# Performance work log

Hardware: AMD Instinct MI355X
Metric: run time of the kernel (lower is better)

## Reference

```python
import jax, jax.numpy as jnp
import numpy as np

NH, WIN = 8, 7  # num_head, window


def _ln(x, w, b, eps=1e-6):
    mu = x.mean(-1, keepdims=True)
    var = ((x - mu) ** 2).mean(-1, keepdims=True)
    return (x - mu) / jnp.sqrt(var + eps) * w + b


def _dwconv(x, w, b):
    # x: (B,C,H,W), w: (C,1,7,7) depthwise, pad 3
    y = jax.lax.conv_general_dilated(
        x, w, (1, 1), ((3, 3), (3, 3)),
        dimension_numbers=('NCHW', 'OIHW', 'NCHW'),
        feature_group_count=x.shape[1])
    return y + b[None, :, None, None]


def _forward(x, x_e, norm_w, norm_b, norme_w, norme_b,
             rr1_w, rr1_b, rr2_w, rr2_b, rr3_w, rr3_b, conv_w, conv_b,
             la1_w, la1_b, la2_w, la2_b, lac1_w, lac1_b, lac2_w, lac2_b,
             fc1_w, fc2_w, la3_w, la3_b,
             kv_w, kv_b, q_w, q_b, proj_w, proj_b, proje_w, proje_b):
    B, H, W, C = x.shape
    hd = C // NH // 2  # head dim of half-width attention
    xn = _ln(x, norm_w, norm_b)
    xen = _ln(x_e, norme_w, norme_b)

    # local_rr branch: gated depthwise-conv mixing (C channels)
    rr1 = xn @ rr1_w + rr1_b
    rr2 = xn @ rr2_w + rr2_b
    rr2 = _dwconv(rr2.transpose(0, 3, 1, 2), conv_w, conv_b).transpose(0, 2, 3, 1)
    rr2 = rr2 @ rr3_w + rr3_b
    local_rr = rr1 * rr2  # (B,H,W,C)

    # LocalAttentionRGBT branch -> (B,H,W,C//2)
    rgb = (xn @ la1_w + la1_b).transpose(0, 3, 1, 2)   # (B,C/2,H,W)
    t = (xen @ la2_w + la2_b).transpose(0, 3, 1, 2)
    co = _dwconv(rgb * t, lac1_w, lac1_b)
    di = _dwconv(jnp.abs(rgb - t), lac2_w, lac2_b)
    co_di = jnp.concatenate([co, di], 1).transpose(0, 2, 3, 1)  # (B,H,W,C)
    amap = co_di.mean(-1, keepdims=True)                         # (B,H,W,1)
    dot = (amap * co_di).sum((1, 2), keepdims=True)              # (B,1,1,C)
    n1 = jnp.sqrt((amap ** 2).sum((1, 2), keepdims=True))        # (B,1,1,1)
    n2 = jnp.sqrt((co_di ** 2).sum((1, 2), keepdims=True))       # (B,1,1,C)
    cos = dot / (n1 * n2 + 1e-6)
    attc = jax.nn.sigmoid(jax.nn.gelu(cos @ fc1_w, approximate=False) @ fc2_w)
    local_rx = (co_di * attc) @ la3_w + la3_b  # (B,H,W,C/2)

    # global pooled attention: 49 queries vs full H*W keys, C/2 wide
    kv = (xn @ kv_w + kv_b).reshape(B, H * W, 2, NH, hd).transpose(2, 0, 3, 1, 4)
    k, v = kv[0], kv[1]  # (B,NH,HW,hd)
    rx = jnp.concatenate([xn, xen], -1)  # (B,H,W,3C/2)
    ph, pw = H // WIN, W // WIN  # exact adaptive pool (H,W divisible by 7)
    rx_pool = rx.reshape(B, WIN, ph, WIN, pw, rx.shape[-1]).mean((2, 4))  # (B,7,7,3C/2)
    q = (rx_pool @ q_w + q_b).reshape(B, WIN * WIN, NH, hd).transpose(0, 2, 1, 3)
    attn = jax.nn.softmax((q * hd ** -0.5) @ k.transpose(0, 1, 3, 2), axis=-1)  # (B,NH,49,HW)
    g = (attn @ v).reshape(B, NH, WIN, WIN, hd).transpose(0, 1, 4, 2, 3).reshape(B, C // 2, WIN, WIN)
    g = jax.image.resize(g, (B, C // 2, H, W), method='bilinear').transpose(0, 2, 3, 1)

    xc = jnp.concatenate([local_rr, g, local_rx], -1)  # (B,H,W,2C)
    out_e = xc @ proje_w + proje_b  # (B,H,W,C/2)
    out = xc @ proj_w + proj_b      # (B,H,W,C)
    return out, out_e


def setup_inputs() -> dict:
    C = 128
    B, H, W = 8, 112, 112
    ks = iter(jax.random.split(jax.random.key(0), 24))

    def w(shape):
        return jax.random.normal(next(ks), shape, jnp.float32) * 0.05

    inp = {
        'x': jax.random.normal(next(ks), (B, H, W, C), jnp.float32),
        'x_e': jax.random.normal(next(ks), (B, H, W, C // 2), jnp.float32),
        'norm_w': jnp.ones((C,), jnp.float32), 'norm_b': jnp.zeros((C,), jnp.float32),
        'norme_w': jnp.ones((C // 2,), jnp.float32), 'norme_b': jnp.zeros((C // 2,), jnp.float32),
        'rr1_w': w((C, C)), 'rr1_b': jnp.zeros((C,), jnp.float32),
        'rr2_w': w((C, C)), 'rr2_b': jnp.zeros((C,), jnp.float32),
        'rr3_w': w((C, C)), 'rr3_b': jnp.zeros((C,), jnp.float32),
        'conv_w': w((C, 1, 7, 7)), 'conv_b': jnp.zeros((C,), jnp.float32),
        'la1_w': w((C, C // 2)), 'la1_b': jnp.zeros((C // 2,), jnp.float32),
        'la2_w': w((C // 2, C // 2)), 'la2_b': jnp.zeros((C // 2,), jnp.float32),
        'lac1_w': w((C // 2, 1, 7, 7)), 'lac1_b': jnp.zeros((C // 2,), jnp.float32),
        'lac2_w': w((C // 2, 1, 7, 7)), 'lac2_b': jnp.zeros((C // 2,), jnp.float32),
        'fc1_w': w((C, C // 8)), 'fc2_w': w((C // 8, C)),
        'la3_w': w((C, C // 2)), 'la3_b': jnp.zeros((C // 2,), jnp.float32),
        'kv_w': w((C, C)), 'kv_b': jnp.zeros((C,), jnp.float32),
        'q_w': w((3 * C // 2, C // 2)), 'q_b': jnp.zeros((C // 2,), jnp.float32),
        'proj_w': w((2 * C, C)), 'proj_b': jnp.zeros((C,), jnp.float32),
        'proje_w': w((2 * C, C // 2)), 'proje_b': jnp.zeros((C // 2,), jnp.float32),
    }
    return inp


def reference(x, x_e, norm_w, norm_b, norme_w, norme_b,
              rr1_w, rr1_b, rr2_w, rr2_b, rr3_w, rr3_b, conv_w, conv_b,
              la1_w, la1_b, la2_w, la2_b, lac1_w, lac1_b, lac2_w, lac2_b,
              fc1_w, fc2_w, la3_w, la3_b,
              kv_w, kv_b, q_w, q_b, proj_w, proj_b, proje_w, proje_b):
    return _forward(x, x_e, norm_w, norm_b, norme_w, norme_b,
                    rr1_w, rr1_b, rr2_w, rr2_b, rr3_w, rr3_b, conv_w, conv_b,
                    la1_w, la1_b, la2_w, la2_b, lac1_w, lac1_b, lac2_w, lac2_b,
                    fc1_w, fc2_w, la3_w, la3_b,
                    kv_w, kv_b, q_w, q_b, proj_w, proj_b, proje_w, proje_b)
```

## Files before the change

### kernel.cpp

```cpp
#include <hip/hip_runtime.h>
#include <math.h>

#define N_POS 100352
#define HW    12544

typedef unsigned short bf16_t;
typedef __attribute__((ext_vector_type(8))) short bf16x8;
typedef __attribute__((ext_vector_type(4))) float f32x4;

__device__ __forceinline__ bf16_t f2b(float f){
  unsigned u = __builtin_bit_cast(unsigned, f);
  unsigned r = (u + 0x7fffu + ((u >> 16) & 1u)) >> 16;
  return (bf16_t)r;
}
__device__ __forceinline__ float b2f(bf16_t h){
  unsigned u = ((unsigned)h) << 16;
  return __builtin_bit_cast(float, u);
}
__device__ __forceinline__ float blo(unsigned u){
  return __builtin_bit_cast(float, u << 16);
}
__device__ __forceinline__ float bhi(unsigned u){
  return __builtin_bit_cast(float, u & 0xffff0000u);
}

__global__ void zero_kernel(float* p, int n){
  int i = blockIdx.x*256 + threadIdx.x;
  if (i < n) p[i] = 0.f;
}

struct WJob { const float* src; bf16_t* dst; int K; int ldw; int n0; };
struct WJobs { WJob j[14]; };
__global__ void wtrans_kernel(WJobs js){
  WJob job = js.j[blockIdx.x];
  int t = threadIdx.x;
  int n = t & 63, k0 = t >> 6;
  for (int k = k0; k < job.K; k += 4)
    job.dst[(size_t)n*job.K + k] = f2b(job.src[(size_t)k*job.ldw + job.n0 + n]);
}

__global__ __launch_bounds__(256) void ln128_kernel(const float* __restrict__ in,
    const float* __restrict__ w, const float* __restrict__ b, bf16_t* __restrict__ out){
  int row  = blockIdx.x*4 + (threadIdx.x >> 6);
  int lane = threadIdx.x & 63;
  const float* p = in + (size_t)row*128;
  float2 v = *(const float2*)(p + lane*2);
  float s = v.x + v.y;
  #pragma unroll
  for (int o = 1; o < 64; o <<= 1) s += __shfl_xor(s, o);
  float mu = s * (1.0f/128.0f);
  float dx = v.x - mu, dy = v.y - mu;
  float q = dx*dx + dy*dy;
  #pragma unroll
  for (int o = 1; o < 64; o <<= 1) q += __shfl_xor(q, o);
  float rs = rsqrtf(q * (1.0f/128.0f) + 1e-6f);
  int c = lane*2;
  ushort2 o2;
  o2.x = f2b(dx*rs*w[c]   + b[c]);
  o2.y = f2b(dy*rs*w[c+1] + b[c+1]);
  *(ushort2*)(out + (size_t)row*128 + c) = o2;
}

__global__ __launch_bounds__(256) void ln64_kernel(const float* __restrict__ in,
    const float* __restrict__ w, const float* __restrict__ b, bf16_t* __restrict__ out){
  int row  = blockIdx.x*4 + (threadIdx.x >> 6);
  int lane = threadIdx.x & 63;
  float v = in[(size_t)row*64 + lane];
  float s = v;
  #pragma unroll
  for (int o = 1; o < 64; o <<= 1) s += __shfl_xor(s, o);
  float mu = s * (1.0f/64.0f);
  float d = v - mu;
  float q = d*d;
  #pragma unroll
  for (int o = 1; o < 64; o <<= 1) q += __shfl_xor(q, o);
  float rs = rsqrtf(q * (1.0f/64.0f) + 1e-6f);
  out[(size_t)row*64 + lane] = f2b(d*rs*w[lane] + b[lane]);
}

struct MTile {
  const bf16_t* Wt;
  const float* bias;
  void* out;
  const bf16_t* mult;
  int ldo; int ldm; int out_fp32;
};
struct MGemmParams {
  const bf16_t* A; const float* scale;
  int lda; int K; int rowsPerB;
  MTile tiles[8];
};

__global__ __launch_bounds__(256) void mgemm(MGemmParams p){
  __shared__ short As[128*72];
  __shared__ short Ws[64*72];
  const int tid = threadIdx.x;
  const MTile tile = p.tiles[blockIdx.x];
  const int row0 = blockIdx.y * 128;
  const int lane = tid & 63, wv = tid >> 6;
  const int wm = wv * 32;
  const int fm = lane & 15;
  const int quad = lane >> 4;
  f32x4 acc[2][4];
  #pragma unroll
  for (int mi = 0; mi < 2; mi++)
    #pragma unroll
    for (int ni = 0; ni < 4; ni++) acc[mi][ni] = (f32x4)0.f;
  const float* scale = p.scale ? (p.scale + (size_t)(row0 / p.rowsPerB) * p.K) : (const float*)0;

  const int sr = tid & 127, sq = tid >> 7;
  const int wn = tid & 63,  wq = tid >> 6;

  for (int k0 = 0; k0 < p.K; k0 += 64) {
    {
      const bf16_t* src = p.A + (size_t)(row0 + sr)*p.lda + k0 + sq*32;
      short* dst = &As[sr*72 + sq*32];
      if (!scale) {
        #pragma unroll
        for (int i = 0; i < 4; i++)
          *(uint4*)(dst + i*8) = *(const uint4*)(src + i*8);
      } else {
        const float* sc = scale + k0 + sq*32;
        #pragma unroll
        for (int i = 0; i < 32; i++) dst[i] = (short)f2b(b2f(src[i]) * sc[i]);
      }
    }
    {
      const bf16_t* src = tile.Wt + (size_t)wn*p.K + k0 + wq*16;
      short* dst = &Ws[wn*72 + wq*16];
      *(uint4*)dst       = *(const uint4*)src;
      *(uint4*)(dst + 8) = *(const uint4*)(src + 8);
    }
    __syncthreads();
    #pragma unroll
    for (int ks = 0; ks < 2; ks++) {
      int kb = ks*32 + quad*8;
      bf16x8 af0 = *(const bf16x8*)&As[(wm + fm)*72 + kb];
      bf16x8 af1 = *(const bf16x8*)&As[(wm + 16 + fm)*72 + kb];
      bf16x8 bfr[4];
      #pragma unroll
      for (int ni = 0; ni < 4; ni++) bfr[ni] = *(const bf16x8*)&Ws[(ni*16 + fm)*72 + kb];
      #pragma unroll
      for (int ni = 0; ni < 4; ni++) {
        acc[0][ni] = __builtin_amdgcn_mfma_f32_16x16x32_bf16(af0, bfr[ni], acc[0][ni], 0, 0, 0);
        acc[1][ni] = __builtin_amdgcn_mfma_f32_16x16x32_bf16(af1, bfr[ni], acc[1][ni], 0, 0, 0);
      }
    }
    __syncthreads();
  }
  #pragma unroll
  for (int mi = 0; mi < 2; mi++) {
    #pragma unroll
    for (int ni = 0; ni < 4; ni++) {
      int col = ni*16 + fm;
      float bias = tile.bias[col];
      #pragma unroll
      for (int r = 0; r < 4; r++) {
        int row = row0 + wm + mi*16 + quad*4 + r;
        float val = acc[mi][ni][r] + bias;
        if (tile.mult) val *= b2f(tile.mult[(size_t)row*tile.ldm + col]);
        if (tile.out_fp32) ((float*)tile.out)[(size_t)row*tile.ldo + col] = val;
        else ((bf16_t*)tile.out)[(size_t)row*tile.ldo + col] = f2b(val);
      }
    }
  }
}

__global__ __launch_bounds__(256) void dwconv128_kernel(const bf16_t* __restrict__ in,
    const float* __restrict__ cw, const float* __restrict__ cb, bf16_t* __restrict__ out){
  __shared__ float wsm[49*128];
  int t = threadIdx.x;
  for (int i = t; i < 6272; i += 256) {
    int ch = i / 49, k = i % 49;
    wsm[k*128 + ch] = cw[i];
  }
  __syncthreads();
  int c = (t & 63) * 2;
  int wv = t >> 6;
  int blk = blockIdx.x;
  int xs = blk % 14; int tmp = blk / 14;
  int yg = tmp % 14; int b = tmp / 14;
  int y0 = yg*8 + wv*2;
  int x0 = xs*8;
  float2 bias; bias.x = cb[c]; bias.y = cb[c+1];
  float2 acc0[8], acc1[8];
  #pragma unroll
  for (int i = 0; i < 8; i++) { acc0[i] = bias; acc1[i] = bias; }
  for (int r = 0; r < 8; r++) {
    int yy = y0 + r - 3;
    if ((unsigned)yy >= 112u) continue;
    const bf16_t* row = in + ((size_t)(b*112+yy)*112)*128 + c;
    unsigned u[14];
    #pragma unroll
    for (int i = 0; i < 14; i++) {
      int xx = x0 + i - 3;
      u[i] = ((unsigned)xx < 112u) ? *(const unsigned*)(row + (size_t)xx*128) : 0u;
    }
    float va[14], vb[14];
    #pragma unroll
    for (int i = 0; i < 14; i++) { va[i] = blo(u[i]); vb[i] = bhi(u[i]); }
    if (r < 7) {
      #pragma unroll
      for (int kx = 0; kx < 7; kx++) {
        float2 w = *(const float2*)&wsm[(r*7+kx)*128 + c];
        #pragma unroll
        for (int i = 0; i < 8; i++) {
          acc0[i].x = fmaf(w.x, va[i+kx], acc0[i].x);
          acc0[i].y = fmaf(w.y, vb[i+kx], acc0[i].y);
        }
      }
    }
    if (r >= 1) {
      #pragma unroll
      for (int kx = 0; kx < 7; kx++) {
        float2 w = *(const float2*)&wsm[((r-1)*7+kx)*128 + c];
        #pragma unroll
        for (int i = 0; i < 8; i++) {
          acc1[i].x = fmaf(w.x, va[i+kx], acc1[i].x);
          acc1[i].y = fmaf(w.y, vb[i+kx], acc1[i].y);
        }
      }
    }
  }
  size_t r0 = (size_t)(b*112+y0)*112 + x0;
  #pragma unroll
  for (int i = 0; i < 8; i++) {
    unsigned o0 = (unsigned)f2b(acc0[i].x) | ((unsigned)f2b(acc0[i].y) << 16);
    unsigned o1 = (unsigned)f2b(acc1[i].x) | ((unsigned)f2b(acc1[i].y) << 16);
    *(unsigned*)(out + (r0+i)*128 + c)       = o0;
    *(unsigned*)(out + (r0+112+i)*128 + c)   = o1;
  }
}

__global__ __launch_bounds__(256) void dwconv_codi_kernel(
    const bf16_t* __restrict__ rgb, const bf16_t* __restrict__ tb,
    const float* __restrict__ w1, const float* __restrict__ b1,
    const float* __restrict__ w2, const float* __restrict__ b2,
    bf16_t* __restrict__ out){
  __shared__ float wsm[49*128];
  int t = threadIdx.x;
  for (int i = t; i < 3136; i += 256) {
    int ch = i / 49, k = i % 49;
    wsm[k*128 + ch]      = w1[i];
    wsm[k*128 + 64 + ch] = w2[i];
  }
  __syncthreads();
  int c = (t & 31) * 2;
  int yrow = t >> 5;
  int blk = blockIdx.x;
  int xs = blk % 14; int tmp = blk / 14;
  int yg = tmp % 14; int b = tmp / 14;
  int y = yg*8 + yrow;
  int x0 = xs*8;
  float2 bco; bco.x = b1[c]; bco.y = b1[c+1];
  float2 bdi; bdi.x = b2[c]; bdi.y = b2[c+1];
  float2 acc_co[8], acc_di[8];
  #pragma unroll
  for (int i = 0; i < 8; i++) { acc_co[i] = bco; acc_di[i] = bdi; }
  for (int r = 0; r < 7; r++) {
    int yy = y + r - 3;
    if ((unsigned)yy >= 112u) continue;
    const bf16_t* rrow = rgb + ((size_t)(b*112+yy)*112)*64 + c;
    const bf16_t* trow = tb  + ((size_t)(b*112+yy)*112)*64 + c;
    unsigned ru[14], tu[14];
    #pragma unroll
    for (int i = 0; i < 14; i++) {
      int xx = x0 + i - 3;
      bool ok = (unsigned)xx < 112u;
      ru[i] = ok ? *(const unsigned*)(rrow + (size_t)xx*64) : 0u;
      tu[i] = ok ? *(const unsigned*)(trow + (size_t)xx*64) : 0u;
    }
    float p0[14], p1[14], d0[14], d1[14];
    #pragma unroll
    for (int i = 0; i < 14; i++) {
      float a0 = blo(ru[i]), a1 = bhi(ru[i]);
      float t0 = blo(tu[i]), t1 = bhi(tu[i]);
      p0[i] = a0*t0; p1[i] = a1*t1;
      d0[i] = fabsf(a0-t0); d1[i] = fabsf(a1-t1);
    }
    #pragma unroll
    for (int kx = 0; kx < 7; kx++) {
      int k = r*7+kx;
      float2 wc = *(const float2*)&wsm[k*128 + c];
      float2 wd = *(const float2*)&wsm[k*128 + 64 + c];
      #pragma unroll
      for (int i = 0; i < 8; i++) {
        acc_co[i].x = fmaf(wc.x, p0[i+kx], acc_co[i].x);
        acc_co[i].y = fmaf(wc.y, p1[i+kx], acc_co[i].y);
        acc_di[i].x = fmaf(wd.x, d0[i+kx], acc_di[i].x);
        acc_di[i].y = fmaf(wd.y, d1[i+kx], acc_di[i].y);
      }
    }
  }
  size_t r0 = (size_t)(b*112+y)*112 + x0;
  #pragma unroll
  for (int i = 0; i < 8; i++) {
    unsigned oc = (unsigned)f2b(acc_co[i].x) | ((unsigned)f2b(acc_co[i].y) << 16);
    unsigned od = (unsigned)f2b(acc_di[i].x) | ((unsigned)f2b(acc_di[i].y) << 16);
    *(unsigned*)(out + (r0+i)*128 + c)      = oc;
    *(unsigned*)(out + (r0+i)*128 + 64 + c) = od;
  }
}

__global__ __launch_bounds__(256) void reduce_kernel(const bf16_t* __restrict__ codi,
    float* __restrict__ dotb, float* __restrict__ n1sq, float* __restrict__ n2sq){
  int blk = blockIdx.x;
  int b = blk / 49, seg = blk % 49;
  int lane = threadIdx.x & 63, w = threadIdx.x >> 6;
  int c = lane*2;
  float d0=0,d1=0,s0=0,s1=0,a1=0;
  for (int i = 0; i < 64; i++) {
    int row = b*HW + seg*256 + w*64 + i;
    ushort2 v2 = *(const ushort2*)(codi + (size_t)row*128 + c);
    float vx = b2f(v2.x), vy = b2f(v2.y);
    float rs = vx + vy;
    #pragma unroll
    for (int o = 1; o < 64; o <<= 1) rs += __shfl_xor(rs, o);
    float amap = rs * (1.0f/128.0f);
    d0 += amap*vx; d1 += amap*vy;
    s0 += vx*vx;   s1 += vy*vy;
    if (lane == 0) a1 += amap*amap;
  }
  atomicAdd(&dotb[b*128+c],   d0); atomicAdd(&dotb[b*128+c+1], d1);
  atomicAdd(&n2sq[b*128+c],   s0); atomicAdd(&n2sq[b*128+c+1], s1);
  if (lane == 0) atomicAdd(&n1sq[b], a1);
}

__global__ __launch_bounds__(128) void attc_kernel(const float* __restrict__ dotb,
    const float* __restrict__ n1sq, const float* __restrict__ n2sq,
    const float* __restrict__ fc1, const float* __restrict__ fc2, float* __restrict__ attc){
  __shared__ float scos[128];
  __shared__ float sh[16];
  int t = threadIdx.x;
  int b = blockIdx.x;
  {
    float n1 = sqrtf(n1sq[b]);
    float n2 = sqrtf(n2sq[b*128+t]);
    scos[t] = dotb[b*128+t] / (n1*n2 + 1e-6f);
  }
  __syncthreads();
  if (t < 16) {
    float h = 0;
    for (int c = 0; c < 128; c++) h += scos[c]*fc1[c*16+t];
    sh[t] = h * 0.5f * (1.0f + erff(h*0.70710678118654752f));
  }
  __syncthreads();
  {
    float a = 0;
    for (int j = 0; j < 16; j++) a += sh[j]*fc2[j*128+t];
    attc[b*128+t] = 1.0f/(1.0f + __expf(-a));
  }
}

__global__ void pool_kernel(const bf16_t* __restrict__ xn, const bf16_t* __restrict__ xen,
                            float* __restrict__ pool){
  int cellb = blockIdx.x;
  int py = blockIdx.y;
  int c = threadIdx.x;
  int b = cellb / 49, cell = cellb % 49;
  int wy = cell / 7, wx = cell % 7;
  float s = 0;
  for (int i = py*2; i < py*2+2; i++)
    for (int j = 0; j < 16; j++) {
      int y = wy*16+i, x = wx*16+j;
      size_t row = (size_t)(b*112+y)*112 + x;
      s += (c < 128) ? b2f(xn[row*128 + c]) : b2f(xen[row*64 + (c-128)]);
    }
  atomicAdd(&pool[(size_t)cellb*192 + c], s);
}

__global__ void qproj_kernel(const float* __restrict__ pool, const float* __restrict__ qw,
                             const float* __restrict__ qb, float* __restrict__ qbuf){
  int cellb = blockIdx.x;
  int j = threadIdx.x;
  float s = qb[j];
  for (int c = 0; c < 192; c++)
    s += pool[(size_t)cellb*192 + c] * (1.0f/256.0f) * qw[c*64 + j];
  qbuf[(size_t)cellb*64 + j] = s * 0.35355339059327373f;
}

__global__ __launch_bounds__(256) void attn_kernel(const float* __restrict__ qbuf,
    const bf16_t* __restrict__ kv, float* __restrict__ part){
  __shared__ float qs[392];
  __shared__ float ks[256*8];
  __shared__ float vs[256*8];
  int t = threadIdx.x;
  int blk = blockIdx.x;
  int b = blk >> 6, nh = (blk >> 3) & 7, sp = blk & 7;
  for (int i = t; i < 392; i += 256)
    qs[i] = qbuf[(size_t)(b*49 + (i>>3))*64 + nh*8 + (i&7)];
  __syncthreads();
  int lane = t & 63, w = t >> 6;
  int qq = lane < 49 ? lane : 0;
  float4 qa = *(const float4*)&qs[qq*8];
  float4 qb4 = *(const float4*)&qs[qq*8+4];
  float m = -1e30f, l = 0.f;
  float4 acca = make_float4(0,0,0,0), accb = make_float4(0,0,0,0);
  const int base = sp * 1568;
  for (int c0 = 0; c0 < 1568; c0 += 256) {
    int cnt = 1568 - c0 < 256 ? 1568 - c0 : 256;
    __syncthreads();
    if (t < cnt) {
      size_t rb = ((size_t)(b*HW + base + c0 + t))*128 + nh*8;
      uint4 kr = *(const uint4*)(kv + rb);
      uint4 vr = *(const uint4*)(kv + rb + 64);
      const bf16_t* kp = (const bf16_t*)&kr;
      const bf16_t* vp = (const bf16_t*)&vr;
      #pragma unroll
      for (int j = 0; j < 8; j++) { ks[t*8+j] = b2f(kp[j]); vs[t*8+j] = b2f(vp[j]); }
    }
    __syncthreads();
    int s0 = w*64;
    int n = cnt - s0; if (n > 64) n = 64;
    for (int i = 0; i < n; i += 16) {
      float s[16];
      #pragma unroll
      for (int j = 0; j < 16; j++) {
        const float* kp = &ks[(s0+i+j)*8];
        float4 ka = *(const float4*)kp, kb = *(const float4*)(kp+4);
        s[j] = qa.x*ka.x + qa.y*ka.y + qa.z*ka.z + qa.w*ka.w
             + qb4.x*kb.x + qb4.y*kb.y + qb4.z*kb.z + qb4.w*kb.w;
      }
      float t8[8];
      #pragma unroll
      for (int j = 0; j < 8; j++) t8[j] = fmaxf(s[2*j], s[2*j+1]);
      float t4a = fmaxf(t8[0], t8[1]), t4b = fmaxf(t8[2], t8[3]);
      float t4c = fmaxf(t8[4], t8[5]), t4d = fmaxf(t8[6], t8[7]);
      float mx = fmaxf(fmaxf(t4a, t4b), fmaxf(t4c, t4d));
      float mn = fmaxf(m, mx);
      float corr = __expf(m - mn);
      float p[16];
      #pragma unroll
      for (int j = 0; j < 16; j++) p[j] = __expf(s[j] - mn);
      float u8[8];
      #pragma unroll
      for (int j = 0; j < 8; j++) u8[j] = p[2*j] + p[2*j+1];
      float u4a = u8[0]+u8[1], u4b = u8[2]+u8[3], u4c = u8[4]+u8[5], u4d = u8[6]+u8[7];
      float lsum = (u4a+u4b) + (u4c+u4d);
      l = fmaf(l, corr, lsum);
      float4 sva = make_float4(0,0,0,0), svb = make_float4(0,0,0,0);
      #pragma unroll
      for (int j = 0; j < 16; j++) {
        const float* vp = &vs[(s0+i+j)*8];
        float4 va = *(const float4*)vp, vb = *(const float4*)(vp+4);
        sva.x = fmaf(p[j], va.x, sva.x); sva.y = fmaf(p[j], va.y, sva.y);
        sva.z = fmaf(p[j], va.z, sva.z); sva.w = fmaf(p[j], va.w, sva.w);
        svb.x = fmaf(p[j], vb.x, svb.x); svb.y = fmaf(p[j], vb.y, svb.y);
        svb.z = fmaf(p[j], vb.z, svb.z); svb.w = fmaf(p[j], vb.w, svb.w);
      }
      acca.x = fmaf(acca.x, corr, sva.x); acca.y = fmaf(acca.y, corr, sva.y);
      acca.z = fmaf(acca.z, corr, sva.z); acca.w = fmaf(acca.w, corr, sva.w);
      accb.x = fmaf(accb.x, corr, svb.x); accb.y = fmaf(accb.y, corr, svb.y);
      accb.z = fmaf(accb.z, corr, svb.z); accb.w = fmaf(accb.w, corr, svb.w);
      m = mn;
    }
  }
  if (lane < 49) {
    size_t idx = ((size_t)(blk*4 + w)*49 + lane)*10;
    part[idx] = m; part[idx+1] = l;
    part[idx+2] = acca.x; part[idx+3] = acca.y; part[idx+4] = acca.z; part[idx+5] = acca.w;
    part[idx+6] = accb.x; part[idx+7] = accb.y; part[idx+8] = accb.z; part[idx+9] = accb.w;
  }
}

__global__ void merge_kernel(const float* __restrict__ part, float* __restrict__ gsm){
  int g = blockIdx.x*64 + threadIdx.x;
  if (g >= 3136) return;
  int b = g / 392, r = g % 392, nh = r / 49, q = r % 49;
  int blkbase = b*64 + nh*8;
  float M = -1e30f;
  for (int sp = 0; sp < 8; sp++)
    for (int w = 0; w < 4; w++) {
      size_t idx = ((size_t)((blkbase+sp)*4 + w)*49 + q)*10;
      M = fmaxf(M, part[idx]);
    }
  float L = 0, a[8] = {0,0,0,0,0,0,0,0};
  for (int sp = 0; sp < 8; sp++)
    for (int w = 0; w < 4; w++) {
      size_t idx = ((size_t)((blkbase+sp)*4 + w)*49 + q)*10;
      float c = __expf(part[idx] - M);
      L += part[idx+1]*c;
      #pragma unroll
      for (int d = 0; d < 8; d++) a[d] += part[idx+2+d]*c;
    }
  #pragma unroll
  for (int d = 0; d < 8; d++)
    gsm[(size_t)(b*49+q)*64 + nh*8 + d] = a[d]/L;
}

__global__ __launch_bounds__(256) void f2_kernel(const float* __restrict__ gsm,
                                                 bf16_t* __restrict__ xc){
  int gidx = blockIdx.x*256 + threadIdx.x;
  int r = gidx >> 6, cc = gidx & 63;
  int b = r / HW, rem = r % HW, y = rem / 112, x = rem % 112;
  float fy = fminf(fmaxf((y + 0.5f)*0.0625f - 0.5f, 0.f), 6.f);
  float fx = fminf(fmaxf((x + 0.5f)*0.0625f - 0.5f, 0.f), 6.f);
  int y0 = (int)fy, x0 = (int)fx;
  float wy = fy - y0, wx = fx - x0;
  int y1 = y0+1 < 6 ? y0+1 : 6, x1 = x0+1 < 6 ? x0+1 : 6;
  const float* gb = gsm + (size_t)b*49*64 + cc;
  float g00 = gb[(y0*7+x0)*64], g01 = gb[(y0*7+x1)*64];
  float g10 = gb[(y1*7+x0)*64], g11 = gb[(y1*7+x1)*64];
  xc[(size_t)r*256 + 128 + cc] =
      f2b((1-wy)*((1-wx)*g00 + wx*g01) + wy*((1-wx)*g10 + wx*g11));
}

extern "C" void kernel_launch(void* const* d_in, const int* in_sizes, int n_in,
                              void* d_out, int out_size, void* d_ws, size_t ws_size,
                              hipStream_t stream) {
  const float* x      = (const float*)d_in[0];
  const float* x_e    = (const float*)d_in[1];
  const float* norm_w = (const float*)d_in[2];
  const float* norm_b = (const float*)d_in[3];
  const float* norme_w= (const float*)d_in[4];
  const float* norme_b= (const float*)d_in[5];
  const float* rr1_w  = (const float*)d_in[6];
  const float* rr1_b  = (const float*)d_in[7];
  const float* rr2_w  = (const float*)d_in[8];
  const float* rr2_b  = (const float*)d_in[9];
  const float* rr3_w  = (const float*)d_in[10];
  const float* rr3_b  = (const float*)d_in[11];
  const float* conv_w = (const float*)d_in[12];
  const float* conv_b = (const float*)d_in[13];
  const float* la1_w  = (const float*)d_in[14];
  const float* la1_b  = (const float*)d_in[15];
  const float* la2_w  = (const float*)d_in[16];
  const float* la2_b  = (const float*)d_in[17];
  const float* lac1_w = (const float*)d_in[18];
  const float* lac1_b = (const float*)d_in[19];
  const float* lac2_w = (const float*)d_in[20];
  const float* lac2_b = (const float*)d_in[21];
  const float* fc1_w  = (const float*)d_in[22];
  const float* fc2_w  = (const float*)d_in[23];
  const float* la3_w  = (const float*)d_in[24];
  const float* la3_b  = (const float*)d_in[25];
  const float* kv_w   = (const float*)d_in[26];
  const float* kv_b   = (const float*)d_in[27];
  const float* q_w    = (const float*)d_in[28];
  const float* q_b    = (const float*)d_in[29];
  const float* proj_w = (const float*)d_in[30];
  const float* proj_b = (const float*)d_in[31];
  const float* proje_w= (const float*)d_in[32];
  const float* proje_b= (const float*)d_in[33];

  const size_t N = N_POS;
  bf16_t* rr1   = (bf16_t*)d_ws;
  bf16_t* xnbuf = rr1 + N*128;
  bf16_t* kvbuf = xnbuf + N*128;
  bf16_t* xcbuf = kvbuf + N*128;
  float* pool = (float*)(xcbuf + N*256);
  float* qbuf = pool + 75264;
  float* part = qbuf + 25088;
  float* gsm  = part + 1003520;
  float* dotb = gsm  + 25088;
  float* n1sq = dotb + 1024;
  float* n2sq = n1sq + 8;
  float* attc = n2sq + 1024;
  bf16_t* wtab = (bf16_t*)(attc + 1024);

  bf16_t* xn = xnbuf;
  bf16_t* convout = xnbuf;
  bf16_t* kv = kvbuf;
  bf16_t* codi = kvbuf;
  bf16_t* rr2a = xcbuf;
  bf16_t* rgb  = xcbuf + N*128;
  bf16_t* xen  = xcbuf + N*192;
  bf16_t* xc   = xcbuf;
  float* outp = (float*)d_out;
  float* oute = outp + N*128;

  bf16_t* rr1t0 = wtab;            bf16_t* rr1t1 = wtab + 8192;
  bf16_t* rr2t0 = wtab + 16384;    bf16_t* rr2t1 = wtab + 24576;
  bf16_t* la1t  = wtab + 32768;
  bf16_t* kvt0  = wtab + 40960;    bf16_t* kvt1  = wtab + 49152;
  bf16_t* la2t  = wtab + 57344;
  bf16_t* rr3t0 = wtab + 61440;    bf16_t* rr3t1 = wtab + 69632;
  bf16_t* la3t  = wtab + 77824;
  bf16_t* projt0= wtab + 86016;    bf16_t* projt1= wtab + 102400;
  bf16_t* projet= wtab + 118784;

  zero_kernel<<<(75264+255)/256, 256, 0, stream>>>(pool, 75264);
  zero_kernel<<<9, 256, 0, stream>>>(dotb, 2056);
  {
    WJobs js;
    js.j[0]  = {rr1_w,  rr1t0, 128, 128,   0};
    js.j[1]  = {rr1_w,  rr1t1, 128, 128,  64};
    js.j[2]  = {rr2_w,  rr2t0, 128, 128,   0};
    js.j[3]  = {rr2_w,  rr2t1, 128, 128,  64};
    js.j[4]  = {la1_w,  la1t,  128,  64,   0};
    js.j[5]  = {kv_w,   kvt0,  128, 128,   0};
    js.j[6]  = {kv_w,   kvt1,  128, 128,  64};
    js.j[7]  = {la2_w,  la2t,   64,  64,   0};
    js.j[8]  = {rr3_w,  rr3t0, 128, 128,   0};
    js.j[9]  = {rr3_w,  rr3t1, 128, 128,  64};
    js.j[10] = {la3_w,  la3t,  128,  64,   0};
    js.j[11] = {proj_w, projt0,256, 128,   0};
    js.j[12] = {proj_w, projt1,256, 128,  64};
    js.j[13] = {proje_w,projet,256,  64,   0};
    wtrans_kernel<<<14, 256, 0, stream>>>(js);
  }
  ln128_kernel<<<N_POS/4, 256, 0, stream>>>(x, norm_w, norm_b, xn);
  ln64_kernel <<<N_POS/4, 256, 0, stream>>>(x_e, norme_w, norme_b, xen);
  pool_kernel<<<dim3(392,8), 192, 0, stream>>>(xn, xen, pool);
  qproj_kernel<<<392, 64, 0, stream>>>(pool, q_w, q_b, qbuf);
  {
    MGemmParams p; p.A = xn; p.scale = 0; p.lda = 128; p.K = 128; p.rowsPerB = HW;
    p.tiles[0] = {rr1t0, rr1_b,    rr1,     0, 128, 0, 0};
    p.tiles[1] = {rr1t1, rr1_b+64, rr1+64,  0, 128, 0, 0};
    p.tiles[2] = {rr2t0, rr2_b,    rr2a,    0, 128, 0, 0};
    p.tiles[3] = {rr2t1, rr2_b+64, rr2a+64, 0, 128, 0, 0};
    p.tiles[4] = {la1t,  la1_b,    rgb,     0,  64, 0, 0};
    p.tiles[5] = {kvt0,  kv_b,     kv,      0, 128, 0, 0};
    p.tiles[6] = {kvt1,  kv_b+64,  kv+64,   0, 128, 0, 0};
    mgemm<<<dim3(7, 784), 256, 0, stream>>>(p);
  }
  attn_kernel<<<512, 256, 0, stream>>>(qbuf, kv, part);
  merge_kernel<<<49, 64, 0, stream>>>(part, gsm);
  {
    MGemmParams p; p.A = xen; p.scale = 0; p.lda = 64; p.K = 64; p.rowsPerB = HW;
    p.tiles[0] = {la2t, la2_b, xen, 0, 64, 0, 0};
    mgemm<<<dim3(1, 784), 256, 0, stream>>>(p);
  }
  dwconv_codi_kernel<<<8*14*14, 256, 0, stream>>>(rgb, xen, lac1_w, lac1_b, lac2_w, lac2_b, codi);
  dwconv128_kernel<<<8*14*14, 256, 0, stream>>>(rr2a, conv_w, conv_b, convout);
  {
    MGemmParams p; p.A = convout; p.scale = 0; p.lda = 128; p.K = 128; p.rowsPerB = HW;
    p.tiles[0] = {rr3t0, rr3_b,    xc,    rr1,    256, 128, 0};
    p.tiles[1] = {rr3t1, rr3_b+64, xc+64, rr1+64, 256, 128, 0};
    mgemm<<<dim3(2, 784), 256, 0, stream>>>(p);
  }
  reduce_kernel<<<392, 256, 0, stream>>>(codi, dotb, n1sq, n2sq);
  attc_kernel<<<8, 128, 0, stream>>>(dotb, n1sq, n2sq, fc1_w, fc2_w, attc);
  {
    MGemmParams p; p.A = codi; p.scale = attc; p.lda = 128; p.K = 128; p.rowsPerB = HW;
    p.tiles[0] = {la3t, la3_b, xc + 192, 0, 256, 0, 0};
    mgemm<<<dim3(1, 784), 256, 0, stream>>>(p);
  }
  f2_kernel<<<25088, 256, 0, stream>>>(gsm, xc);
  {
    MGemmParams p; p.A = xc; p.scale = 0; p.lda = 256; p.K = 256; p.rowsPerB = HW;
    p.tiles[0] = {projt0, proj_b,    outp,    0, 128, 0, 1};
    p.tiles[1] = {projt1, proj_b+64, outp+64, 0, 128, 0, 1};
    p.tiles[2] = {projet, proje_b,   oute,    0,  64, 0, 1};
    mgemm<<<dim3(3, 784), 256, 0, stream>>>(p);
  }
}
```

Baseline: 632.4 us.

## Remap mgemm blocks for XCD locality and split attention across more blocks

```diff
diff --git a/kernel.cpp b/kernel.cpp
--- a/kernel.cpp
+++ b/kernel.cpp
@@ -87,7 +87,7 @@
 };
 struct MGemmParams {
   const bf16_t* A; const float* scale;
-  int lda; int K; int rowsPerB;
+  int lda; int K; int rowsPerB; int ntiles;
   MTile tiles[8];
 };
 
@@ -95,8 +95,13 @@
   __shared__ short As[128*72];
   __shared__ short Ws[64*72];
   const int tid = threadIdx.x;
-  const MTile tile = p.tiles[blockIdx.x];
-  const int row0 = blockIdx.y * 128;
+  const int bid = blockIdx.x;
+  const int xcd = bid & 7;
+  const int j = bid >> 3;
+  const int ti = j % p.ntiles;
+  const int rb = (j / p.ntiles) * 8 + xcd;
+  const MTile tile = p.tiles[ti];
+  const int row0 = rb * 128;
   const int lane = tid & 63, wv = tid >> 6;
   const int wm = wv * 32;
   const int fm = lane & 15;
@@ -386,7 +391,7 @@
   __shared__ float vs[256*8];
   int t = threadIdx.x;
   int blk = blockIdx.x;
-  int b = blk >> 6, nh = (blk >> 3) & 7, sp = blk & 7;
+  int b = blk >> 7, nh = (blk >> 4) & 7, sp = blk & 15;
   for (int i = t; i < 392; i += 256)
     qs[i] = qbuf[(size_t)(b*49 + (i>>3))*64 + nh*8 + (i&7)];
   __syncthreads();
@@ -396,22 +401,38 @@
   float4 qb4 = *(const float4*)&qs[qq*8+4];
   float m = -1e30f, l = 0.f;
   float4 acca = make_float4(0,0,0,0), accb = make_float4(0,0,0,0);
-  const int base = sp * 1568;
-  for (int c0 = 0; c0 < 1568; c0 += 256) {
-    int cnt = 1568 - c0 < 256 ? 1568 - c0 : 256;
+  const int base = sp * 784;
+  uint4 kr, vr;
+  {
+    size_t rb = ((size_t)(b*HW + base + t))*128 + nh*8;
+    kr = *(const uint4*)(kv + rb);
+    vr = *(const uint4*)(kv + rb + 64);
+  }
+  for (int c0 = 0; c0 < 784; c0 += 256) {
+    int cnt = 784 - c0 < 256 ? 784 - c0 : 256;
     __syncthreads();
     if (t < cnt) {
-      size_t rb = ((size_t)(b*HW + base + c0 + t))*128 + nh*8;
-      uint4 kr = *(const uint4*)(kv + rb);
-      uint4 vr = *(const uint4*)(kv + rb + 64);
       const bf16_t* kp = (const bf16_t*)&kr;
       const bf16_t* vp = (const bf16_t*)&vr;
-      #pragma unroll
-      for (int j = 0; j < 8; j++) { ks[t*8+j] = b2f(kp[j]); vs[t*8+j] = b2f(vp[j]); }
+      float4 k0 = make_float4(b2f(kp[0]), b2f(kp[1]), b2f(kp[2]), b2f(kp[3]));
+      float4 k1 = make_float4(b2f(kp[4]), b2f(kp[5]), b2f(kp[6]), b2f(kp[7]));
+      float4 v0 = make_float4(b2f(vp[0]), b2f(vp[1]), b2f(vp[2]), b2f(vp[3]));
+      float4 v1 = make_float4(b2f(vp[4]), b2f(vp[5]), b2f(vp[6]), b2f(vp[7]));
+      *(float4*)&ks[t*8]   = k0; *(float4*)&ks[t*8+4] = k1;
+      *(float4*)&vs[t*8]   = v0; *(float4*)&vs[t*8+4] = v1;
     }
     __syncthreads();
+    int c1 = c0 + 256;
+    if (c1 < 784) {
+      int cnt1 = 784 - c1 < 256 ? 784 - c1 : 256;
+      if (t < cnt1) {
+        size_t rb = ((size_t)(b*HW + base + c1 + t))*128 + nh*8;
+        kr = *(const uint4*)(kv + rb);
+        vr = *(const uint4*)(kv + rb + 64);
+      }
+    }
     int s0 = w*64;
-    int n = cnt - s0; if (n > 64) n = 64;
+    int n = cnt - s0; if (n < 0) n = 0; if (n > 64) n = 64;
     for (int i = 0; i < n; i += 16) {
       float s[16];
       #pragma unroll
@@ -455,11 +476,31 @@
       m = mn;
     }
   }
+  __syncthreads();
   if (lane < 49) {
-    size_t idx = ((size_t)(blk*4 + w)*49 + lane)*10;
-    part[idx] = m; part[idx+1] = l;
-    part[idx+2] = acca.x; part[idx+3] = acca.y; part[idx+4] = acca.z; part[idx+5] = acca.w;
-    part[idx+6] = accb.x; part[idx+7] = accb.y; part[idx+8] = accb.z; part[idx+9] = accb.w;
+    float* rp = &vs[((size_t)w*49 + lane)*10];
+    rp[0] = m; rp[1] = l;
+    rp[2] = acca.x; rp[3] = acca.y; rp[4] = acca.z; rp[5] = acca.w;
+    rp[6] = accb.x; rp[7] = accb.y; rp[8] = accb.z; rp[9] = accb.w;
+  }
+  __syncthreads();
+  if (t < 49) {
+    float M = -1e30f;
+    #pragma unroll
+    for (int w4 = 0; w4 < 4; w4++) M = fmaxf(M, vs[(w4*49 + t)*10]);
+    float L = 0, a[8] = {0,0,0,0,0,0,0,0};
+    #pragma unroll
+    for (int w4 = 0; w4 < 4; w4++) {
+      const float* rp = &vs[(w4*49 + t)*10];
+      float c = __expf(rp[0] - M);
+      L += rp[1]*c;
+      #pragma unroll
+      for (int d = 0; d < 8; d++) a[d] += rp[2+d]*c;
+    }
+    size_t idx = ((size_t)blk*49 + t)*10;
+    part[idx] = M; part[idx+1] = L;
+    #pragma unroll
+    for (int d = 0; d < 8; d++) part[idx+2+d] = a[d];
   }
 }
 
@@ -467,22 +508,18 @@
   int g = blockIdx.x*64 + threadIdx.x;
   if (g >= 3136) return;
   int b = g / 392, r = g % 392, nh = r / 49, q = r % 49;
-  int blkbase = b*64 + nh*8;
+  int blkbase = b*128 + nh*16;
   float M = -1e30f;
-  for (int sp = 0; sp < 8; sp++)
-    for (int w = 0; w < 4; w++) {
-      size_t idx = ((size_t)((blkbase+sp)*4 + w)*49 + q)*10;
-      M = fmaxf(M, part[idx]);
-    }
+  for (int sp = 0; sp < 16; sp++)
+    M = fmaxf(M, part[((size_t)(blkbase+sp)*49 + q)*10]);
   float L = 0, a[8] = {0,0,0,0,0,0,0,0};
-  for (int sp = 0; sp < 8; sp++)
-    for (int w = 0; w < 4; w++) {
-      size_t idx = ((size_t)((blkbase+sp)*4 + w)*49 + q)*10;
-      float c = __expf(part[idx] - M);
-      L += part[idx+1]*c;
-      #pragma unroll
-      for (int d = 0; d < 8; d++) a[d] += part[idx+2+d]*c;
-    }
+  for (int sp = 0; sp < 16; sp++) {
+    size_t idx = ((size_t)(blkbase+sp)*49 + q)*10;
+    float c = __expf(part[idx] - M);
+    L += part[idx+1]*c;
+    #pragma unroll
+    for (int d = 0; d < 8; d++) a[d] += part[idx+2+d]*c;
+  }
   #pragma unroll
   for (int d = 0; d < 8; d++)
     gsm[(size_t)(b*49+q)*64 + nh*8 + d] = a[d]/L;
@@ -604,7 +641,7 @@
   pool_kernel<<<dim3(392,8), 192, 0, stream>>>(xn, xen, pool);
   qproj_kernel<<<392, 64, 0, stream>>>(pool, q_w, q_b, qbuf);
   {
-    MGemmParams p; p.A = xn; p.scale = 0; p.lda = 128; p.K = 128; p.rowsPerB = HW;
+    MGemmParams p; p.A = xn; p.scale = 0; p.lda = 128; p.K = 128; p.rowsPerB = HW; p.ntiles = 7;
     p.tiles[0] = {rr1t0, rr1_b,    rr1,     0, 128, 0, 0};
     p.tiles[1] = {rr1t1, rr1_b+64, rr1+64,  0, 128, 0, 0};
     p.tiles[2] = {rr2t0, rr2_b,    rr2a,    0, 128, 0, 0};
@@ -612,36 +649,36 @@
     p.tiles[4] = {la1t,  la1_b,    rgb,     0,  64, 0, 0};
     p.tiles[5] = {kvt0,  kv_b,     kv,      0, 128, 0, 0};
     p.tiles[6] = {kvt1,  kv_b+64,  kv+64,   0, 128, 0, 0};
-    mgemm<<<dim3(7, 784), 256, 0, stream>>>(p);
-  }
-  attn_kernel<<<512, 256, 0, stream>>>(qbuf, kv, part);
+    mgemm<<<8*7*98, 256, 0, stream>>>(p);
+  }
+  attn_kernel<<<1024, 256, 0, stream>>>(qbuf, kv, part);
   merge_kernel<<<49, 64, 0, stream>>>(part, gsm);
   {
-    MGemmParams p; p.A = xen; p.scale = 0; p.lda = 64; p.K = 64; p.rowsPerB = HW;
+    MGemmParams p; p.A = xen; p.scale = 0; p.lda = 64; p.K = 64; p.rowsPerB = HW; p.ntiles = 1;
     p.tiles[0] = {la2t, la2_b, xen, 0, 64, 0, 0};
-    mgemm<<<dim3(1, 784), 256, 0, stream>>>(p);
+    mgemm<<<8*1*98, 256, 0, stream>>>(p);
   }
   dwconv_codi_kernel<<<8*14*14, 256, 0, stream>>>(rgb, xen, lac1_w, lac1_b, lac2_w, lac2_b, codi);
   dwconv128_kernel<<<8*14*14, 256, 0, stream>>>(rr2a, conv_w, conv_b, convout);
   {
-    MGemmParams p; p.A = convout; p.scale = 0; p.lda = 128; p.K = 128; p.rowsPerB = HW;
+    MGemmParams p; p.A = convout; p.scale = 0; p.lda = 128; p.K = 128; p.rowsPerB = HW; p.ntiles = 2;
     p.tiles[0] = {rr3t0, rr3_b,    xc,    rr1,    256, 128, 0};
     p.tiles[1] = {rr3t1, rr3_b+64, xc+64, rr1+64, 256, 128, 0};
-    mgemm<<<dim3(2, 784), 256, 0, stream>>>(p);
+    mgemm<<<8*2*98, 256, 0, stream>>>(p);
   }
   reduce_kernel<<<392, 256, 0, stream>>>(codi, dotb, n1sq, n2sq);
   attc_kernel<<<8, 128, 0, stream>>>(dotb, n1sq, n2sq, fc1_w, fc2_w, attc);
   {
-    MGemmParams p; p.A = codi; p.scale = attc; p.lda = 128; p.K = 128; p.rowsPerB = HW;
+    MGemmParams p; p.A = codi; p.scale = attc; p.lda = 128; p.K = 128; p.rowsPerB = HW; p.ntiles = 1;
     p.tiles[0] = {la3t, la3_b, xc + 192, 0, 256, 0, 0};
-    mgemm<<<dim3(1, 784), 256, 0, stream>>>(p);
+    mgemm<<<8*1*98, 256, 0, stream>>>(p);
   }
   f2_kernel<<<25088, 256, 0, stream>>>(gsm, xc);
   {
-    MGemmParams p; p.A = xc; p.scale = 0; p.lda = 256; p.K = 256; p.rowsPerB = HW;
+    MGemmParams p; p.A = xc; p.scale = 0; p.lda = 256; p.K = 256; p.rowsPerB = HW; p.ntiles = 3;
     p.tiles[0] = {projt0, proj_b,    outp,    0, 128, 0, 1};
     p.tiles[1] = {projt1, proj_b+64, outp+64, 0, 128, 0, 1};
     p.tiles[2] = {projet, proje_b,   oute,    0,  64, 0, 1};
-    mgemm<<<dim3(3, 784), 256, 0, stream>>>(p);
-  }
-}
+    mgemm<<<8*3*98, 256, 0, stream>>>(p);
+  }
+}
```

Measured after the change: 606.9 us. 1.04x faster.
